# Kernel optimization log

Measured on AMD Instinct MI355X. Metric: run time of the kernel, lower is better.

Reference implementation:

```python
import jax, jax.numpy as jnp
import numpy as np
from jax import lax


def setup_inputs() -> dict:
    key = jax.random.key(0)
    ks = jax.random.split(key, 8)
    B, L, H = 2, 1024, 2048
    E = 2
    d = H * E            # d_inner = 4096
    S = 16               # state_dim
    R = 128              # dt_rank = ceil(H / 16)
    sc = lambda fan_in: 1.0 / np.sqrt(fan_in)
    return {
        "x": jax.random.normal(ks[0], (B, L, H), jnp.float32),
        "W_in": jax.random.normal(ks[1], (H, 2 * d), jnp.float32) * sc(H),
        "conv_w": jax.random.normal(ks[2], (d, 1, 3), jnp.float32) * sc(3),
        "conv_b": jnp.zeros((d,), jnp.float32),
        "W_x": jax.random.normal(ks[3], (d, R + 2 * S), jnp.float32) * sc(d),
        "W_dt": jax.random.normal(ks[4], (R, d), jnp.float32) * sc(R),
        "b_dt": jnp.zeros((d,), jnp.float32),
        "A_log": jnp.log(jnp.tile(jnp.arange(1, S + 1, dtype=jnp.float32), (d, 1))),
        "D": jnp.ones((d,), jnp.float32),
        "W_out": jax.random.normal(ks[5], (d, H), jnp.float32) * sc(d),
    }


def reference(x, W_in, conv_w, conv_b, W_x, W_dt, b_dt, A_log, D, W_out):
    d = conv_b.shape[0]
    S = A_log.shape[1]
    R = W_dt.shape[0]
    # in_proj and gate split
    xz = x @ W_in                              # [B, L, 2d]
    xp, z = jnp.split(xz, 2, axis=-1)          # each [B, L, d]
    # depthwise conv1d (kernel 3, pad 1)
    xc = lax.conv_general_dilated(
        jnp.transpose(xp, (0, 2, 1)), conv_w, (1,), [(1, 1)],
        feature_group_count=d, dimension_numbers=("NCH", "OIH", "NCH"))
    xc = jnp.transpose(xc + conv_b[None, :, None], (0, 2, 1))  # [B, L, d]
    xc = jax.nn.silu(xc)
    # x_proj -> dt, B, C
    x_dbl = xc @ W_x                           # [B, L, R + 2S]
    dt_in = x_dbl[..., :R]
    Bm = x_dbl[..., R:R + S]                   # [B, L, S]
    Cm = x_dbl[..., R + S:]                    # [B, L, S]
    dt = jax.nn.softplus(dt_in @ W_dt + b_dt)  # [B, L, d]
    A = -jnp.exp(A_log)                        # [d, S]

    def step(h, ins):
        u_t, dt_t, B_t, C_t = ins              # [B,d], [B,d], [B,S], [B,S]
        dA = jnp.exp(dt_t[:, :, None] * A)     # [B, d, S]
        h = dA * h + dt_t[:, :, None] * B_t[:, None, :] * u_t[:, :, None]
        y_t = jnp.einsum("bds,bs->bd", h, C_t)
        return h, y_t

    h0 = jnp.zeros((x.shape[0], d, S), xc.dtype)
    xsT = (jnp.swapaxes(xc, 0, 1), jnp.swapaxes(dt, 0, 1),
           jnp.swapaxes(Bm, 0, 1), jnp.swapaxes(Cm, 0, 1))
    _, yT = lax.scan(step, h0, xsT)            # yT: [L, B, d]
    y = jnp.swapaxes(yT, 0, 1) + xc * D        # skip connection
    y = y * jax.nn.silu(z)                     # gate
    return y @ W_out                           # [B, L, H]
```

## Files before the change

kernel.cpp:

```cpp
#include <hip/hip_runtime.h>
#include <hip/hip_bf16.h>


using u16 = unsigned short;
typedef __bf16 bf16x8 __attribute__((ext_vector_type(8)));
typedef float f32x4 __attribute__((ext_vector_type(4)));

#define NCHUNK 16
#define CLEN   64
#define SWZ(row, q) ((q) ^ (((row) >> 1) & 3))

__device__ __forceinline__ float bf2f(u16 u) {
    union { unsigned int i; float f; } v; v.i = ((unsigned int)u) << 16; return v.f;
}
__device__ __forceinline__ u16 f2bf(float f) {
    union { float f; unsigned int i; } v; v.f = f;
    unsigned int x = v.i;
    return (u16)((x + 0x7FFFu + ((x >> 16) & 1u)) >> 16);
}

__device__ __forceinline__ float* hloc_ptr(u16* xzbase, int i) {
    return reinterpret_cast<float*>(xzbase + (size_t)(i >> 11) * 8192) + (i & 2047);
}
__device__ __forceinline__ float* hin_ptr(u16* xzbase, int i) {
    return reinterpret_cast<float*>(xzbase + (size_t)((i >> 11) + 1024) * 8192) + (i & 2047);
}

__global__ void detect_dtype(const u16* __restrict__ xraw, int* __restrict__ flag) {
    __shared__ int cnt[256];
    const int tid = threadIdx.x;
    int plausible = 0;
    for (int i = tid; i < 4096; i += 256) {
        const u16 v = xraw[2 * i];
        const int e = (v >> 7) & 0xFF;
        plausible += (e >= 100 && e <= 145) ? 1 : 0;
    }
    cnt[tid] = plausible;
    __syncthreads();
    for (int s = 128; s > 0; s >>= 1) {
        if (tid < s) cnt[tid] += cnt[tid + s];
        __syncthreads();
    }
    if (tid == 0) *flag = (cnt[0] > 2458) ? 1 : 0;
}

__device__ __forceinline__ void cvt_seg(const void* src, u16* dst, int i,
                                        bool isbf) {
    dst[i] = isbf ? ((const u16*)src)[i] : f2bf(((const float*)src)[i]);
}
__global__ void cvt_fused(const void* __restrict__ x_raw, u16* __restrict__ xcan,
                          const void* __restrict__ cw_raw, u16* __restrict__ cw_c,
                          const void* __restrict__ cb_raw, u16* __restrict__ cb_c,
                          const void* __restrict__ bdt_raw, u16* __restrict__ bdt_c,
                          const void* __restrict__ Alog_raw, u16* __restrict__ Alog_c,
                          const void* __restrict__ D_raw, u16* __restrict__ D_c,
                          float* __restrict__ x_dbl,
                          const int* __restrict__ flag) {
    const bool isbf = (*flag != 0);
    int blk = blockIdx.x;
    const int tid = threadIdx.x;
    if (blk < 16384) { cvt_seg(x_raw, xcan, blk * 256 + tid, isbf); return; }
    blk -= 16384;
    if (blk < 48)  { cvt_seg(cw_raw, cw_c, blk * 256 + tid, isbf); return; }
    blk -= 48;
    if (blk < 16)  { cvt_seg(cb_raw, cb_c, blk * 256 + tid, isbf); return; }
    blk -= 16;
    if (blk < 16)  { cvt_seg(bdt_raw, bdt_c, blk * 256 + tid, isbf); return; }
    blk -= 16;
    if (blk < 256) { cvt_seg(Alog_raw, Alog_c, blk * 256 + tid, isbf); return; }
    blk -= 256;
    if (blk < 16)  { cvt_seg(D_raw, D_c, blk * 256 + tid, isbf); return; }
    blk -= 16;
    x_dbl[blk * 256 + tid] = 0.f;
}

__device__ __forceinline__ void tr_tile(const void* in, u16* out, int R, int C,
                                        int bx, int by, int tx, int ty, bool isbf,
                                        u16 (*tile)[33]) {
    const int c0 = bx * 32, r0 = by * 32;
#pragma unroll
    for (int i = 0; i < 4; i++) {
        const size_t idx = (size_t)(r0 + ty + i * 8) * C + c0 + tx;
        tile[ty + i * 8][tx] = isbf ? ((const u16*)in)[idx]
                                    : f2bf(((const float*)in)[idx]);
    }
    __syncthreads();
#pragma unroll
    for (int i = 0; i < 4; i++)
        out[(size_t)(c0 + ty + i * 8) * R + r0 + tx] = tile[tx][ty + i * 8];
}
__global__ void transpose_fused(const void* __restrict__ Wi, u16* __restrict__ WiT,
                                const void* __restrict__ Wo, u16* __restrict__ WoT,
                                const void* __restrict__ Wd, u16* __restrict__ WdT,
                                const void* __restrict__ Wx, u16* __restrict__ WxT,
                                const int* __restrict__ flag) {
    __shared__ u16 tile[32][33];
    const bool isbf = (*flag != 0);
    const int tx = threadIdx.x, ty = threadIdx.y;
    int blk = blockIdx.x;
    if (blk < 16384) { tr_tile(Wi, WiT, 2048, 8192, blk % 256, blk / 256, tx, ty, isbf, tile); return; }
    blk -= 16384;
    if (blk < 8192)  { tr_tile(Wo, WoT, 4096, 2048, blk % 64, blk / 64, tx, ty, isbf, tile); return; }
    blk -= 8192;
    if (blk < 512)   { tr_tile(Wd, WdT, 128, 4096, blk % 128, blk / 128, tx, ty, isbf, tile); return; }
    blk -= 512;
    tr_tile(Wx, WxT, 4096, 160, blk % 5, blk / 5, tx, ty, isbf, tile);
}

template <int BM, int BN, int BK, int WR, int WC, int MT, int NT, int MODE>
__global__ __launch_bounds__(256) void gemm_bt(
    const u16* __restrict__ A, const u16* __restrict__ Bt,
    void* __restrict__ C, const u16* __restrict__ bias,
    const int* __restrict__ oflagp,
    int M, int N, int K)
{
    static_assert(BK == 32, "BK=32 (one 16x16x32 MFMA k-slab)");
    __shared__ u16 As[BM * BK];
    __shared__ u16 Bs[BN * BK];

    const int tid  = threadIdx.x;
    const int lane = tid & 63;
    const int wave = tid >> 6;
    const int wm = wave / WC, wn = wave % WC;

    const int m0 = blockIdx.y * BM;
    const int n0 = blockIdx.x * BN;
    const int Kchunk = K / gridDim.z;
    const int kbeg = blockIdx.z * Kchunk;
    const int kend = kbeg + Kchunk;

    int oflag = 1;
    if constexpr (MODE == 1) oflag = *oflagp;

    f32x4 acc[MT][NT];
#pragma unroll
    for (int mi = 0; mi < MT; mi++)
#pragma unroll
        for (int ni = 0; ni < NT; ni++)
            acc[mi][ni] = (f32x4){0.f, 0.f, 0.f, 0.f};

    const int q = lane >> 4;
    const int arow = wm * MT * 16 + (lane & 15);
    const int brow = wn * NT * 16 + (lane & 15);

    constexpr int CHA = BM * 4;
    constexpr int CHB = BN * 4;

    for (int k0 = kbeg; k0 < kend; k0 += BK) {
        __syncthreads();
#pragma unroll
        for (int it = 0; it < (CHA + 255) / 256; it++) {
            const int c = it * 256 + tid;
            if (CHA % 256 == 0 || c < CHA) {
                const int row = c >> 2, kc = SWZ(row, c & 3);
                const u16* gp = &A[(size_t)(m0 + row) * K + k0 + kc * 8];
                __builtin_amdgcn_global_load_lds(
                    (const __attribute__((address_space(1))) void*)gp,
                    (__attribute__((address_space(3))) void*)&As[c * 8], 16, 0, 0);
            }
        }
#pragma unroll
        for (int it = 0; it < (CHB + 255) / 256; it++) {
            const int c = it * 256 + tid;
            if (CHB % 256 == 0 || c < CHB) {
                const int row = c >> 2, kc = SWZ(row, c & 3);
                const u16* gp = &Bt[(size_t)(n0 + row) * K + k0 + kc * 8];
                __builtin_amdgcn_global_load_lds(
                    (const __attribute__((address_space(1))) void*)gp,
                    (__attribute__((address_space(3))) void*)&Bs[c * 8], 16, 0, 0);
            }
        }
        __syncthreads();

        bf16x8 af[MT], bfr[NT];
#pragma unroll
        for (int mi = 0; mi < MT; mi++) {
            const int row = arow + mi * 16;
            af[mi] = *reinterpret_cast<const bf16x8*>(&As[row * BK + SWZ(row, q) * 8]);
        }
#pragma unroll
        for (int ni = 0; ni < NT; ni++) {
            const int row = brow + ni * 16;
            bfr[ni] = *reinterpret_cast<const bf16x8*>(&Bs[row * BK + SWZ(row, q) * 8]);
        }
#pragma unroll
        for (int mi = 0; mi < MT; mi++)
#pragma unroll
            for (int ni = 0; ni < NT; ni++)
                acc[mi][ni] = __builtin_amdgcn_mfma_f32_16x16x32_bf16(
                    af[mi], bfr[ni], acc[mi][ni], 0, 0, 0);
    }

    const int rb = m0 + wm * MT * 16 + ((lane >> 4) << 2);
    const int cb = n0 + wn * NT * 16 + (lane & 15);
#pragma unroll
    for (int mi = 0; mi < MT; mi++) {
#pragma unroll
        for (int ni = 0; ni < NT; ni++) {
            const int col = cb + ni * 16;
#pragma unroll
            for (int r = 0; r < 4; r++) {
                const int row = rb + mi * 16 + r;
                const float v = acc[mi][ni][r];
                if constexpr (MODE == 0) {
                    ((u16*)C)[(size_t)row * N + col] = f2bf(v);
                } else if constexpr (MODE == 1) {
                    if (oflag) ((u16*)C)[(size_t)row * N + col] = f2bf(v);
                    else       ((float*)C)[(size_t)row * N + col] = v;
                } else if constexpr (MODE == 4) {
                    atomicAdd(((float*)C) + (size_t)row * N + col, v);
                }
            }
        }
    }
}

__global__ __launch_bounds__(256) void dt_gemm(
    const u16* __restrict__ A,
    const u16* __restrict__ Bt,
    float* __restrict__ C,
    const u16* __restrict__ bias)
{
    __shared__ ulong4 smem_raw[2048];
    u16* As = (u16*)smem_raw;
    u16* Bs = As + 64 * 128;
    float* Cs = (float*)smem_raw;

    const int tid  = threadIdx.x;
    const int lane = tid & 63;
    const int wave = tid >> 6;
    const int n0 = blockIdx.x * 64;
    const int m0 = blockIdx.y * 64;

#pragma unroll
    for (int it = 0; it < 4; it++) {
        const int c = it * 256 + tid;
        const int row = c >> 4, cc = (c & 15) ^ (row & 7);
        const u16* gp = &A[(size_t)(m0 + row) * 128 + cc * 8];
        __builtin_amdgcn_global_load_lds(
            (const __attribute__((address_space(1))) void*)gp,
            (__attribute__((address_space(3))) void*)&As[c * 8], 16, 0, 0);
    }
#pragma unroll
    for (int it = 0; it < 4; it++) {
        const int c = it * 256 + tid;
        const int row = c >> 4, cc = (c & 15) ^ (row & 7);
        const u16* gp = &Bt[(size_t)(n0 + row) * 128 + cc * 8];
        __builtin_amdgcn_global_load_lds(
            (const __attribute__((address_space(1))) void*)gp,
            (__attribute__((address_space(3))) void*)&Bs[c * 8], 16, 0, 0);
    }
    __syncthreads();

    const int q  = lane >> 4;
    const int ar = wave * 16 + (lane & 15);
    f32x4 acc[4];
#pragma unroll
    for (int ni = 0; ni < 4; ni++) acc[ni] = (f32x4){0.f, 0.f, 0.f, 0.f};

#pragma unroll
    for (int kk = 0; kk < 4; kk++) {
        const int cA = kk * 4 + q;
        const bf16x8 af = *reinterpret_cast<const bf16x8*>(
            &As[(ar * 16 + (cA ^ (ar & 7))) * 8]);
#pragma unroll
        for (int ni = 0; ni < 4; ni++) {
            const int br = ni * 16 + (lane & 15);
            const bf16x8 bfr = *reinterpret_cast<const bf16x8*>(
                &Bs[(br * 16 + (cA ^ (br & 7))) * 8]);
            acc[ni] = __builtin_amdgcn_mfma_f32_16x16x32_bf16(af, bfr, acc[ni], 0, 0, 0);
        }
    }
    __syncthreads();

#pragma unroll
    for (int ni = 0; ni < 4; ni++) {
        const int col = ni * 16 + (lane & 15);
#pragma unroll
        for (int r = 0; r < 4; r++) {
            const int rowl = wave * 16 + q * 4 + r;
            Cs[rowl * 68 + col] = acc[ni][r];
        }
    }
    __syncthreads();

#pragma unroll
    for (int p = 0; p < 4; p++) {
        const int rowl = p * 16 + (tid >> 4);
        const int c0 = (tid & 15) * 4;
        float4 v = *reinterpret_cast<const float4*>(&Cs[rowl * 68 + c0]);
        float* vp = reinterpret_cast<float*>(&v);
#pragma unroll
        for (int j = 0; j < 4; j++) {
            const float x = vp[j] + bf2f(bias[n0 + c0 + j]);
            vp[j] = fmaxf(x, 0.f) + __logf(1.f + __expf(-fabsf(x)));
        }
        *reinterpret_cast<float4*>(&C[(size_t)(m0 + rowl) * 4096 + n0 + c0]) = v;
    }
}

__global__ void conv_silu(const u16* __restrict__ xz, const u16* __restrict__ conv_w,
                          const u16* __restrict__ conv_b, u16* __restrict__ xc) {
    const int idx = blockIdx.x * 256 + threadIdx.x;
    const int row = idx >> 12, c = idx & 4095;
    const int l = row & 1023;
    const float w0 = bf2f(conv_w[c * 3 + 0]);
    const float w1 = bf2f(conv_w[c * 3 + 1]);
    const float w2 = bf2f(conv_w[c * 3 + 2]);
    const float x0 = bf2f(xz[(size_t)row * 8192 + c]);
    const float xm = (l > 0)    ? bf2f(xz[(size_t)(row - 1) * 8192 + c]) : 0.f;
    const float xp = (l < 1023) ? bf2f(xz[(size_t)(row + 1) * 8192 + c]) : 0.f;
    float v = w0 * xm + w1 * x0 + w2 * xp + bf2f(conv_b[c]);
    v = v / (1.f + __expf(-v));
    xc[(size_t)row * 4096 + c] = f2bf(v);
}

__global__ void cvt_dtin(const float* __restrict__ x_dbl, u16* __restrict__ dtin) {
    const int idx = blockIdx.x * 256 + threadIdx.x;
    const int row = idx >> 7, c = idx & 127;
    dtin[idx] = f2bf(x_dbl[(size_t)row * 160 + c]);
}

__global__ __launch_bounds__(256) void scan_p1(
    const float* __restrict__ dt, const u16* __restrict__ xc,
    const float* __restrict__ x_dbl, const u16* __restrict__ A_log,
    float* __restrict__ Parr, u16* __restrict__ xzbase)
{
    __shared__ float Bsm[CLEN][16];
    const int tid = threadIdx.x;
    const int nc = blockIdx.x, cg = blockIdx.y, b = blockIdx.z;
    const int ch = cg * 256 + tid;
    const size_t row0 = (size_t)b * 1024 + nc * CLEN;

    {
        const int t = tid >> 2, q = tid & 3;
        const float4 v = *(const float4*)&x_dbl[(row0 + t) * 160 + 128 + q * 4];
        *(float4*)&Bsm[t][q * 4] = v;
    }
    __syncthreads();

    float A_s[16], h[16];
#pragma unroll
    for (int s = 0; s < 16; s++) {
        A_s[s] = -__expf(bf2f(A_log[ch * 16 + s]));
        h[s] = 0.f;
    }
    float Sdt = 0.f;

    float dt_v = dt[row0 * 4096 + ch];
    float u_v  = bf2f(xc[row0 * 4096 + ch]);
    for (int t = 0; t < CLEN; t++) {
        const int tn = (t + 1 < CLEN) ? t + 1 : t;
        const float dt_n = dt[(row0 + tn) * 4096 + ch];
        const float u_n  = bf2f(xc[(row0 + tn) * 4096 + ch]);
        const float dtu = dt_v * u_v;
        Sdt += dt_v;
        const f32x4* Brow = (const f32x4*)&Bsm[t][0];
        const f32x4 B0 = Brow[0], B1 = Brow[1], B2 = Brow[2], B3 = Brow[3];
#pragma unroll
        for (int s = 0; s < 16; s++) {
            const float Bs_ = (s < 4 ? B0[s & 3] : s < 8 ? B1[s & 3] : s < 12 ? B2[s & 3] : B3[s & 3]);
            const float dA = __expf(dt_v * A_s[s]);
            h[s] = dA * h[s] + dtu * Bs_;
        }
        dt_v = dt_n; u_v = u_n;
    }
    const int i0 = (((b * NCHUNK + nc) * 4096) + ch) * 16;
#pragma unroll
    for (int s = 0; s < 16; s++) {
        Parr[i0 + s] = __expf(A_s[s] * Sdt);
        *hloc_ptr(xzbase, i0 + s) = h[s];
    }
}

__global__ __launch_bounds__(256) void scan_p2(
    const float* __restrict__ Parr, u16* __restrict__ xzbase)
{
    const int tid = threadIdx.x;
    const int lane = tid & 63, wave = tid >> 6;
    const int blk = blockIdx.x;
    const int b = blk >> 8, cg = blk & 255;
    const int c_local = lane & 3, s = lane >> 2;
    const int ch = cg * 16 + wave * 4 + c_local;

    float Pv[NCHUNK], hl[NCHUNK];
#pragma unroll
    for (int c = 0; c < NCHUNK; c++) {
        const int i = (((b * NCHUNK + c) * 4096) + ch) * 16 + s;
        Pv[c] = Parr[i];
        hl[c] = *hloc_ptr(xzbase, i);
    }
    float hin = 0.f;
#pragma unroll
    for (int c = 0; c < NCHUNK; c++) {
        const int i = (((b * NCHUNK + c) * 4096) + ch) * 16 + s;
        *hin_ptr(xzbase, i) = hin;
        hin = Pv[c] * hin + hl[c];
    }
}

__global__ __launch_bounds__(256) void scan_p3(
    const float* __restrict__ dt, const u16* __restrict__ xc,
    const float* __restrict__ x_dbl, const u16* __restrict__ xz,
    const u16* __restrict__ A_log, const u16* __restrict__ Dp,
    u16* __restrict__ yg, u16* __restrict__ xzbase)
{
    __shared__ float BCs[CLEN][32];
    const int tid = threadIdx.x;
    const int nc = blockIdx.x, cg = blockIdx.y, b = blockIdx.z;
    const int ch = cg * 256 + tid;
    const size_t row0 = (size_t)b * 1024 + nc * CLEN;

#pragma unroll
    for (int it = 0; it < 2; it++) {
        const int c = it * 256 + tid;
        const int t = c >> 3, q = c & 7;
        const float4 v = *(const float4*)&x_dbl[(row0 + t) * 160 + 128 + q * 4];
        *(float4*)&BCs[t][q * 4] = v;
    }
    __syncthreads();

    float A_s[16], h[16];
    const int i0 = (((b * NCHUNK + nc) * 4096) + ch) * 16;
#pragma unroll
    for (int s = 0; s < 16; s++) {
        A_s[s] = -__expf(bf2f(A_log[ch * 16 + s]));
        h[s] = *hin_ptr(xzbase, i0 + s);
    }
    const float D_ch = bf2f(Dp[ch]);

    float dt_v = dt[row0 * 4096 + ch];
    float u_v  = bf2f(xc[row0 * 4096 + ch]);
    float z_v  = bf2f(xz[row0 * 8192 + 4096 + ch]);
    for (int t = 0; t < CLEN; t++) {
        const int tn = (t + 1 < CLEN) ? t + 1 : t;
        const size_t rn = row0 + tn;
        const float dt_n = dt[rn * 4096 + ch];
        const float u_n  = bf2f(xc[rn * 4096 + ch]);
        const float z_n  = bf2f(xz[rn * 8192 + 4096 + ch]);
        const float dtu = dt_v * u_v;

        const f32x4* Row = (const f32x4*)&BCs[t][0];
        const f32x4 B0 = Row[0], B1 = Row[1], B2 = Row[2], B3 = Row[3];
        const f32x4 C0 = Row[4], C1 = Row[5], C2 = Row[6], C3 = Row[7];

        float y0 = 0.f, y1 = 0.f, y2 = 0.f, y3 = 0.f;
#pragma unroll
        for (int s = 0; s < 16; s++) {
            const float Bs_ = (s < 4 ? B0[s & 3] : s < 8 ? B1[s & 3] : s < 12 ? B2[s & 3] : B3[s & 3]);
            const float Cs_ = (s < 4 ? C0[s & 3] : s < 8 ? C1[s & 3] : s < 12 ? C2[s & 3] : C3[s & 3]);
            const float dA = __expf(dt_v * A_s[s]);
            h[s] = dA * h[s] + dtu * Bs_;
            const float hc = h[s] * Cs_;
            if ((s & 3) == 0) y0 += hc; else if ((s & 3) == 1) y1 += hc;
            else if ((s & 3) == 2) y2 += hc; else y3 += hc;
        }
        const float y = (y0 + y1) + (y2 + y3);
        const float silu_z = z_v / (1.f + __expf(-z_v));
        yg[(row0 + t) * 4096 + ch] = f2bf((y + u_v * D_ch) * silu_z);
        dt_v = dt_n; u_v = u_n; z_v = z_n;
    }
}

extern "C" void kernel_launch(void* const* d_in, const int* in_sizes, int n_in,
                              void* d_out, int out_size, void* d_ws, size_t ws_size,
                              hipStream_t stream)
{
    const void* x_raw      = d_in[0];
    const void* W_in_raw   = d_in[1];
    const void* conv_w_raw = d_in[2];
    const void* conv_b_raw = d_in[3];
    const void* W_x_raw    = d_in[4];
    const void* W_dt_raw   = d_in[5];
    const void* b_dt_raw   = d_in[6];
    const void* A_log_raw  = d_in[7];
    const void* D_raw      = d_in[8];
    const void* W_out_raw  = d_in[9];

    char* ws = (char*)d_ws;
    size_t off = 0;
    auto alloc = [&](size_t bytes) { char* p = ws + off; off += (bytes + 255) & ~(size_t)255; return p; };
    int*   flag   = (int*)  alloc(4);
    u16*   W_inT  = (u16*)  alloc(8192ULL * 2048 * 2);
    u16*   W_outT = (u16*)  alloc(2048ULL * 4096 * 2);
    u16*   W_dtT  = (u16*)  alloc(4096ULL * 128 * 2);
    u16*   W_xT   = (u16*)  alloc(160ULL * 4096 * 2);
    u16*   xz     = (u16*)  alloc(2048ULL * 8192 * 2);
    u16*   xc     = (u16*)  alloc(2048ULL * 4096 * 2);
    float* x_dbl  = (float*)alloc(2048ULL * 160 * 4);
    u16*   dtin   = (u16*)  alloc(2048ULL * 128 * 2);
    u16*   yg     = (u16*)  alloc(2048ULL * 4096 * 2);
    u16*   xcan   = (u16*)  alloc(2048ULL * 2048 * 2);
    u16*   cw_c   = (u16*)  alloc(12288 * 2);
    u16*   cb_c   = (u16*)  alloc(4096 * 2);
    u16*   bdt_c  = (u16*)  alloc(4096 * 2);
    u16*   Alog_c = (u16*)  alloc(65536 * 2);
    u16*   D_c    = (u16*)  alloc(4096 * 2);
    float* dtv    = (float*)W_inT;
    float* Parr   = (float*)xcan;

    detect_dtype<<<1, 256, 0, stream>>>((const u16*)x_raw, flag);
    cvt_fused<<<16384 + 48 + 16 + 16 + 256 + 16 + 1280, 256, 0, stream>>>(
        x_raw, xcan, conv_w_raw, cw_c, conv_b_raw, cb_c, b_dt_raw, bdt_c,
        A_log_raw, Alog_c, D_raw, D_c, x_dbl, flag);

    transpose_fused<<<16384 + 8192 + 512 + 640, dim3(32, 8), 0, stream>>>(
        W_in_raw, W_inT, W_out_raw, W_outT, W_dt_raw, W_dtT, W_x_raw, W_xT, flag);

    gemm_bt<128, 128, 32, 2, 2, 4, 4, 0>
        <<<dim3(8192 / 128, 2048 / 128, 1), 256, 0, stream>>>(xcan, W_inT, xz, nullptr, nullptr, 2048, 8192, 2048);

    conv_silu<<<(2048 * 4096) / 256, 256, 0, stream>>>(xz, cw_c, cb_c, xc);

    gemm_bt<64, 160, 32, 4, 1, 1, 10, 4>
        <<<dim3(1, 2048 / 64, 8), 256, 0, stream>>>(xc, W_xT, x_dbl, nullptr, nullptr, 2048, 160, 4096);

    cvt_dtin<<<(2048 * 128) / 256, 256, 0, stream>>>(x_dbl, dtin);

    dt_gemm<<<dim3(4096 / 64, 2048 / 64), 256, 0, stream>>>(dtin, W_dtT, dtv, bdt_c);

    scan_p1<<<dim3(NCHUNK, 16, 2), 256, 0, stream>>>(dtv, xc, x_dbl, Alog_c, Parr, xz);
    scan_p2<<<512, 256, 0, stream>>>(Parr, xz);
    scan_p3<<<dim3(NCHUNK, 16, 2), 256, 0, stream>>>(dtv, xc, x_dbl, xz, Alog_c, D_c, yg, xz);

    gemm_bt<64, 128, 32, 2, 2, 2, 4, 1>
        <<<dim3(2048 / 128, 2048 / 64, 1), 256, 0, stream>>>(yg, W_outT, d_out, nullptr, flag, 2048, 2048, 4096);
}
```

Baseline: 507.7 us.

## Replace in_proj GEMM with 256x256 tile, 4-stage direct-to-LDS pipelined kernel

New measurement: 474.0 us. 1.07x faster.

```diff
diff --git a/kernel.cpp b/kernel.cpp
--- a/kernel.cpp
+++ b/kernel.cpp
@@ -107,6 +107,113 @@
     tr_tile(Wx, WxT, 4096, 160, blk % 5, blk / 5, tx, ty, isbf, tile);
 }
 
+__device__ __forceinline__ void stage256(const u16* __restrict__ Ab,
+                                         const u16* __restrict__ Bb,
+                                         int K, int k0, u16* dst, int tid)
+{
+#pragma unroll
+    for (int it = 0; it < 2; it++) {
+        const int c = it * 512 + tid;
+        const int row = c >> 2, kc = SWZ(row, c & 3);
+        __builtin_amdgcn_global_load_lds(
+            (const __attribute__((address_space(1))) void*)(Ab + (size_t)row * K + k0 + kc * 8),
+            (__attribute__((address_space(3))) void*)(dst + c * 8), 16, 0, 0);
+    }
+#pragma unroll
+    for (int it = 0; it < 2; it++) {
+        const int c = it * 512 + tid;
+        const int row = c >> 2, kc = SWZ(row, c & 3);
+        __builtin_amdgcn_global_load_lds(
+            (const __attribute__((address_space(1))) void*)(Bb + (size_t)row * K + k0 + kc * 8),
+            (__attribute__((address_space(3))) void*)(dst + 8192 + c * 8), 16, 0, 0);
+    }
+}
+
+__global__ __launch_bounds__(512, 2) void gemm256(
+    const u16* __restrict__ A, const u16* __restrict__ Bt, u16* __restrict__ C,
+    int M, int N, int K)
+{
+    extern __shared__ u16 smem[];
+    const int tid  = threadIdx.x;
+    const int lane = tid & 63;
+    const int wave = tid >> 6;
+    const int wm = wave >> 2, wn = wave & 3;
+    const int q  = lane >> 4;
+    const int n0 = blockIdx.x * 256;
+    const int m0 = blockIdx.y * 256;
+    const int NT = K >> 5;
+
+    const u16* Ab = A  + (size_t)m0 * K;
+    const u16* Bb = Bt + (size_t)n0 * K;
+
+    stage256(Ab, Bb, K, 0,  smem + 0 * 16384, tid);
+    stage256(Ab, Bb, K, 32, smem + 1 * 16384, tid);
+    stage256(Ab, Bb, K, 64, smem + 2 * 16384, tid);
+
+    f32x4 acc[8][4];
+#pragma unroll
+    for (int mi = 0; mi < 8; mi++)
+#pragma unroll
+        for (int ni = 0; ni < 4; ni++)
+            acc[mi][ni] = (f32x4){0.f, 0.f, 0.f, 0.f};
+
+    const int arow = wm * 128 + (lane & 15);
+    const int brow = wn * 64  + (lane & 15);
+
+    for (int t = 0; t < NT; t++) {
+        const int tp = t + 3;
+        if (tp < NT) {
+            stage256(Ab, Bb, K, tp * 32, smem + (tp & 3) * 16384, tid);
+            asm volatile("s_waitcnt vmcnt(12)" ::: "memory");
+        } else if (tp == NT) {
+            asm volatile("s_waitcnt vmcnt(8)" ::: "memory");
+        } else if (tp == NT + 1) {
+            asm volatile("s_waitcnt vmcnt(4)" ::: "memory");
+        } else {
+            asm volatile("s_waitcnt vmcnt(0)" ::: "memory");
+        }
+        __builtin_amdgcn_s_barrier();
+
+        const u16* As = smem + (t & 3) * 16384;
+        const u16* Bs = As + 8192;
+        bf16x8 af[8], bfr[4];
+#pragma unroll
+        for (int mi = 0; mi < 8; mi++) {
+            const int r = arow + mi * 16;
+            af[mi] = *reinterpret_cast<const bf16x8*>(&As[r * 32 + SWZ(r, q) * 8]);
+        }
+#pragma unroll
+        for (int ni = 0; ni < 4; ni++) {
+            const int r = brow + ni * 16;
+            bfr[ni] = *reinterpret_cast<const bf16x8*>(&Bs[r * 32 + SWZ(r, q) * 8]);
+        }
+        __builtin_amdgcn_s_setprio(1);
+#pragma unroll
+        for (int mi = 0; mi < 8; mi++)
+#pragma unroll
+            for (int ni = 0; ni < 4; ni++)
+                acc[mi][ni] = __builtin_amdgcn_mfma_f32_16x16x32_bf16(
+                    af[mi], bfr[ni], acc[mi][ni], 0, 0, 0);
+        __builtin_amdgcn_s_setprio(0);
+
+        __builtin_amdgcn_sched_barrier(0);
+        __builtin_amdgcn_s_barrier();
+    }
+
+    const int rb = m0 + wm * 128 + (q << 2);
+    const int cb = n0 + wn * 64 + (lane & 15);
+#pragma unroll
+    for (int mi = 0; mi < 8; mi++) {
+#pragma unroll
+        for (int ni = 0; ni < 4; ni++) {
+            const int col = cb + ni * 16;
+#pragma unroll
+            for (int r = 0; r < 4; r++)
+                C[(size_t)(rb + mi * 16 + r) * N + col] = f2bf(acc[mi][ni][r]);
+        }
+    }
+}
+
 template <int BM, int BN, int BK, int WR, int WC, int MT, int NT, int MODE>
 __global__ __launch_bounds__(256) void gemm_bt(
     const u16* __restrict__ A, const u16* __restrict__ Bt,
@@ -507,8 +614,10 @@
     transpose_fused<<<16384 + 8192 + 512 + 640, dim3(32, 8), 0, stream>>>(
         W_in_raw, W_inT, W_out_raw, W_outT, W_dt_raw, W_dtT, W_x_raw, W_xT, flag);
 
-    gemm_bt<128, 128, 32, 2, 2, 4, 4, 0>
-        <<<dim3(8192 / 128, 2048 / 128, 1), 256, 0, stream>>>(xcan, W_inT, xz, nullptr, nullptr, 2048, 8192, 2048);
+    (void)hipFuncSetAttribute(reinterpret_cast<const void*>(gemm256),
+                              hipFuncAttributeMaxDynamicSharedMemorySize, 131072);
+    gemm256<<<dim3(8192 / 256, 2048 / 256), 512, 131072, stream>>>(
+        xcan, W_inT, xz, 2048, 8192, 2048);
 
     conv_silu<<<(2048 * 4096) / 256, 256, 0, stream>>>(xz, cw_c, cb_c, xc);
 
```
